# Performance work log

Hardware: AMD Instinct MI355X
Metric: run time of the kernel (lower is better)

## Reference

```python
import jax, jax.numpy as jnp
import numpy as np

B, L, DIM, HEADS = 2, 2048, 1536, 12
HD = DIM // HEADS  # 128
C = HD // 2        # 64 rotary pairs
EPS = 1e-6


def setup_inputs() -> dict:
    key = jax.random.key(0)
    ks = jax.random.split(key, 8)
    x = jax.random.normal(ks[0], (B, L, DIM), jnp.float32)
    # ragged grids: sample0 fills L, sample1 has 2*24*32 = 1536 valid tokens
    grid_sizes = jnp.array([[2, 32, 32], [2, 24, 32]], dtype=jnp.int32)
    seq_lens = jnp.array([2048, 1536], dtype=jnp.int32)
    # rope freqs table [1024, C] (cos/sin of pos * inv_freq)
    pos = jnp.arange(1024, dtype=jnp.float32)[:, None]
    inv = 1.0 / (10000.0 ** (jnp.arange(C, dtype=jnp.float32) / C))
    ang = pos * inv
    freqs_cos, freqs_sin = jnp.cos(ang), jnp.sin(ang)
    init = lambda k: jax.random.normal(k, (DIM, DIM), jnp.float32) / np.sqrt(DIM)
    return dict(
        x=x, seq_lens=seq_lens, grid_sizes=grid_sizes,
        freqs_cos=freqs_cos, freqs_sin=freqs_sin,
        Wq=init(ks[1]), bq=jnp.zeros((DIM,), jnp.float32),
        Wk=init(ks[2]), bk=jnp.zeros((DIM,), jnp.float32),
        Wv=init(ks[3]), bv=jnp.zeros((DIM,), jnp.float32),
        Wo=init(ks[4]), bo=jnp.zeros((DIM,), jnp.float32),
        gq=jnp.ones((DIM,), jnp.float32), gk=jnp.ones((DIM,), jnp.float32),
    )


def _rope_one(xb, grid, cos, sin):
    # xb: [L, n, d]; grid: (f, h, w); cos/sin: [1024, C]
    f, h, w = grid[0], grid[1], grid[2]
    c = cos.shape[1]
    c2 = c // 3
    c1 = c - 2 * c2  # freqs split [c1, c2, c2] over axes (f, h, w)
    p = jnp.arange(xb.shape[0])
    hw = h * w
    valid = p < f * hw
    fi = jnp.where(valid, p // hw, 0)
    hi = jnp.where(valid, (p // w) % h, 0)
    wi = jnp.where(valid, p % w, 0)
    cos_p = jnp.concatenate([cos[fi, :c1], cos[hi, c1:c1 + c2], cos[wi, c1 + c2:]], axis=-1)
    sin_p = jnp.concatenate([sin[fi, :c1], sin[hi, c1:c1 + c2], sin[wi, c1 + c2:]], axis=-1)
    # positions beyond seq_len pass through unrotated (identity rotation)
    cos_p = jnp.where(valid[:, None], cos_p, 1.0)[:, None, :]  # [L,1,C]
    sin_p = jnp.where(valid[:, None], sin_p, 0.0)[:, None, :]
    xr, xi = xb[..., 0::2], xb[..., 1::2]
    out_r = xr * cos_p - xi * sin_p
    out_i = xr * sin_p + xi * cos_p
    return jnp.stack([out_r, out_i], axis=-1).reshape(xb.shape)


_rope_apply = jax.vmap(_rope_one, in_axes=(0, 0, None, None))


def _rms(t, g):
    t32 = t.astype(jnp.float32)
    return (t32 * jax.lax.rsqrt(jnp.mean(t32 * t32, axis=-1, keepdims=True) + EPS) * g).astype(t.dtype)


def reference(x, seq_lens, grid_sizes, freqs_cos, freqs_sin,
              Wq, bq, Wk, bk, Wv, bv, Wo, bo, gq, gk):
    b, s = x.shape[:2]
    n, d = HEADS, HD
    q = _rms(x @ Wq + bq, gq).reshape(b, s, n, d)
    k = _rms(x @ Wk + bk, gk).reshape(b, s, n, d)
    v = (x @ Wv + bv).reshape(b, s, n, d)
    q = _rope_apply(q, grid_sizes, freqs_cos, freqs_sin)
    k = _rope_apply(k, grid_sizes, freqs_cos, freqs_sin)
    scale = 1.0 / np.sqrt(d).astype(np.float32)
    scores = jnp.einsum('bqnd,bknd->bnqk', q, k) * scale
    kmask = jnp.arange(s)[None, :] < seq_lens[:, None]  # [b, s] key validity
    scores = jnp.where(kmask[:, None, None, :], scores, jnp.float32(-1e9))
    attn = jax.nn.softmax(scores, axis=-1)
    out = jnp.einsum('bnqk,bknd->bqnd', attn, v).reshape(b, s, n * d)
    return out @ Wo + bo
```

## Files before the change

kernel.cpp:

```cpp
#include <hip/hip_runtime.h>
#include <hip/hip_bf16.h>

#define DIM   1536
#define HEADS 12
#define HD    128
#define LSEQ  2048
#define NB    2
#define NTOK  (NB*LSEQ)

using f32x4  = __attribute__((ext_vector_type(4))) float;
using f32x16 = __attribute__((ext_vector_type(16))) float;
using s16x8  = __attribute__((ext_vector_type(8))) short;
using u16x4  = __attribute__((ext_vector_type(4))) unsigned short;

__device__ __forceinline__ unsigned short f2bf(float f) {
  unsigned int u = __builtin_bit_cast(unsigned int, f);
  u += 0x7fffu + ((u >> 16) & 1u);
  return (unsigned short)(u >> 16);
}
__device__ __forceinline__ float bf2f(unsigned short u) {
  return __builtin_bit_cast(float, (unsigned int)u << 16);
}
__device__ __forceinline__ unsigned pk2(float a, float b) {
  unsigned r;
  asm("v_cvt_pk_bf16_f32 %0, %1, %2" : "=v"(r) : "v"(a), "v"(b));
  return r;
}
__device__ __forceinline__ unsigned long long pack4bf(float a, float b, float c, float d) {
  return (unsigned long long)f2bf(a) | ((unsigned long long)f2bf(b) << 16) |
         ((unsigned long long)f2bf(c) << 32) | ((unsigned long long)f2bf(d) << 48);
}
__device__ __forceinline__ void plswap(unsigned &x, unsigned &y) {
  asm volatile("v_permlane32_swap_b32 %0, %1" : "+v"(x), "+v"(y));
}
__device__ __forceinline__ void gload_lds16(const void* g, void* l) {
  __builtin_amdgcn_global_load_lds(
      (__attribute__((address_space(1))) void*)const_cast<void*>(g),
      (__attribute__((address_space(3))) void*)l,
      16, 0, 0);
}

__global__ __launch_bounds__(256) void prep(
    const float* __restrict__ x, unsigned short* __restrict__ xb,
    const float* __restrict__ W0, const float* __restrict__ W1,
    const float* __restrict__ W2, const float* __restrict__ W3,
    unsigned short* __restrict__ Wt) {
  __shared__ unsigned short t[64][68];
  const int bid = blockIdx.x;
  const int tid = threadIdx.x;
  if (bid < 2304) {
    const int z = bid / 576, rem = bid % 576;
    const float* W = z == 0 ? W0 : z == 1 ? W1 : z == 2 ? W2 : W3;
    unsigned short* out = Wt + (size_t)z * DIM * DIM;
    const int n0 = (rem % 24) * 64, k0 = (rem / 24) * 64;
#pragma unroll
    for (int i = 0; i < 16; i++) {
      int idx = tid + i * 256;
      int r = idx >> 6, c = idx & 63;
      t[r][c] = f2bf(W[(size_t)(k0 + r) * DIM + n0 + c]);
    }
    __syncthreads();
#pragma unroll
    for (int i = 0; i < 16; i++) {
      int idx = tid + i * 256;
      int r = idx >> 6, c = idx & 63;
      out[(size_t)(n0 + r) * DIM + k0 + c] = t[c][r];
    }
  } else {
    int i = ((bid - 2304) * 256 + tid) * 4;
    int stride = 1024 * 256 * 4;
    for (; i < NTOK * DIM; i += stride) {
      f32x4 v = *(const f32x4*)(x + i);
      u16x4 o;
      o[0] = f2bf(v[0]); o[1] = f2bf(v[1]); o[2] = f2bf(v[2]); o[3] = f2bf(v[3]);
      *(u16x4*)(xb + i) = o;
    }
  }
}

__global__ __launch_bounds__(256) void gemm_bt(
    const unsigned short* __restrict__ A, const unsigned short* __restrict__ Bt,
    void* __restrict__ Cv,
    const float* __restrict__ b0, const float* __restrict__ b1, const float* __restrict__ b2,
    int M, int N, int K, int biasMode, int outBf16) {
  __shared__ __align__(16) unsigned short As[128 * 64];
  __shared__ __align__(16) unsigned short Bs[128 * 64];
  const int tid = threadIdx.x;
  const int lane = tid & 63, w = tid >> 6;
  const int wr = w >> 1, wc = w & 1;
  const int l15 = lane & 15, g4 = lane >> 4;
  const int nwg = gridDim.x * gridDim.y;
  const int bidf = blockIdx.y * gridDim.x + blockIdx.x;
  const int cpx = nwg >> 3;
  const int sw = (bidf & 7) * cpx + (bidf >> 3);
  const int m0 = (sw / gridDim.x) * 128, n0 = (sw % gridDim.x) * 128;

  f32x4 acc[4][4];
#pragma unroll
  for (int i = 0; i < 4; i++)
#pragma unroll
    for (int j = 0; j < 4; j++) acc[i][j] = (f32x4){0.f, 0.f, 0.f, 0.f};

  for (int kt = 0; kt < K; kt += 64) {
    __syncthreads();
#pragma unroll
    for (int i = 0; i < 4; i++) {
      int c = tid + i * 256;
      int row = c >> 3, g = c & 7;
      int gs = g ^ (row & 7);
      gload_lds16(A + (size_t)(m0 + row) * K + kt + gs * 8, As + c * 8);
    }
#pragma unroll
    for (int i = 0; i < 4; i++) {
      int c = tid + i * 256;
      int row = c >> 3, g = c & 7;
      int gs = g ^ (row & 7);
      gload_lds16(Bt + (size_t)(n0 + row) * K + kt + gs * 8, Bs + c * 8);
    }
    __syncthreads();
#pragma unroll
    for (int kk = 0; kk < 2; kk++) {
      s16x8 af[4], bfr[4];
#pragma unroll
      for (int m = 0; m < 4; m++) {
        int row = wr * 64 + m * 16 + l15;
        int off = row * 128 + ((kk * 64 + g4 * 16) ^ ((row & 7) << 4));
        af[m] = *(const s16x8*)((const char*)As + off);
      }
#pragma unroll
      for (int n = 0; n < 4; n++) {
        int row = wc * 64 + n * 16 + l15;
        int off = row * 128 + ((kk * 64 + g4 * 16) ^ ((row & 7) << 4));
        bfr[n] = *(const s16x8*)((const char*)Bs + off);
      }
#pragma unroll
      for (int m = 0; m < 4; m++)
#pragma unroll
        for (int n = 0; n < 4; n++)
          acc[m][n] = __builtin_amdgcn_mfma_f32_16x16x32_bf16(af[m], bfr[n], acc[m][n], 0, 0, 0);
    }
  }
#pragma unroll
  for (int m = 0; m < 4; m++)
#pragma unroll
    for (int n = 0; n < 4; n++)
#pragma unroll
      for (int r = 0; r < 4; r++) {
        int grow = m0 + wr * 64 + m * 16 + g4 * 4 + r;
        int gcol = n0 + wc * 64 + n * 16 + l15;
        float bias = (biasMode == 1)
                         ? b0[gcol]
                         : (gcol < 1536 ? b0[gcol]
                                        : (gcol < 3072 ? b1[gcol - 1536] : b2[gcol - 3072]));
        float val = acc[m][n][r] + bias;
        if (outBf16) ((unsigned short*)Cv)[(size_t)grow * N + gcol] = f2bf(val);
        else         ((float*)Cv)[(size_t)grow * N + gcol] = val;
      }
}

__global__ __launch_bounds__(256) void rmsv(
    const unsigned short* __restrict__ qkvb,
    const float* __restrict__ gq, const float* __restrict__ gk,
    const int* __restrict__ grid_sizes,
    const float* __restrict__ fcos, const float* __restrict__ fsin,
    unsigned short* __restrict__ qb, unsigned short* __restrict__ kb,
    unsigned short* __restrict__ vt) {
  __shared__ float qrow[1536], krow[1536];
  __shared__ float red[8];
  __shared__ unsigned short tile[64][130];
  const int tid = threadIdx.x;
  if (blockIdx.x < 4096) {
    const int t = blockIdx.x;
    const int b = t >> 11, l = t & 2047;
    const unsigned short* rq = qkvb + (size_t)t * 4608;
    const unsigned short* rk = rq + 1536;
    float sq = 0.f, sk = 0.f;
    if (tid < 192) {
      s16x8 vq = *(const s16x8*)(rq + tid * 8);
      s16x8 vk = *(const s16x8*)(rk + tid * 8);
#pragma unroll
      for (int j = 0; j < 8; j++) {
        float a = bf2f((unsigned short)vq[j]); qrow[tid * 8 + j] = a; sq += a * a;
        float c = bf2f((unsigned short)vk[j]); krow[tid * 8 + j] = c; sk += c * c;
      }
    }
    for (int o = 32; o; o >>= 1) { sq += __shfl_down(sq, o); sk += __shfl_down(sk, o); }
    if ((tid & 63) == 0) { red[tid >> 6] = sq; red[4 + (tid >> 6)] = sk; }
    __syncthreads();
    const float rsq = rsqrtf((red[0] + red[1] + red[2] + red[3]) * (1.f / 1536.f) + 1e-6f);
    const float rsk = rsqrtf((red[4] + red[5] + red[6] + red[7]) * (1.f / 1536.f) + 1e-6f);
    const float QS = 0.08838834764831845f * 1.4426950408889634f;
    const int fg = grid_sizes[b * 3 + 0], hg = grid_sizes[b * 3 + 1], wg = grid_sizes[b * 3 + 2];
    const int hw = hg * wg;
    const bool valid = l < fg * hw;
    const int fi = valid ? l / hw : 0;
    const int hi = valid ? (l / wg) % hg : 0;
    const int wi = valid ? l % wg : 0;
    const size_t obase = (((size_t)b * HEADS) * LSEQ + l) * HD;
    for (int i = tid; i < HEADS * 64; i += 256) {
      int hd = i >> 6, j = i & 63;
      float c, s;
      if (valid) {
        int idx = j < 22 ? fi : (j < 43 ? hi : wi);
        c = fcos[idx * 64 + j]; s = fsin[idx * 64 + j];
      } else { c = 1.f; s = 0.f; }
      int col = hd * 128 + 2 * j;
      size_t o = obase + (size_t)hd * LSEQ * HD + 2 * j;
      float xr = qrow[col] * rsq * gq[col];
      float xi = qrow[col + 1] * rsq * gq[col + 1];
      float q0 = (xr * c - xi * s) * QS, q1 = (xr * s + xi * c) * QS;
      *(unsigned int*)(qb + o) = (unsigned int)f2bf(q0) | ((unsigned int)f2bf(q1) << 16);
      xr = krow[col] * rsk * gk[col];
      xi = krow[col + 1] * rsk * gk[col + 1];
      *(unsigned int*)(kb + o) =
          (unsigned int)f2bf(xr * c - xi * s) | ((unsigned int)f2bf(xr * s + xi * c) << 16);
    }
  } else {
    const int r = blockIdx.x - 4096;
    const int lt = r & 31, hb = r >> 5;
    const int h = hb % 12, b = hb / 12;
    const int l0 = lt * 64;
#pragma unroll
    for (int i = 0; i < 4; i++) {
      int idx = tid + i * 256;
      int tk = idx >> 4, dc = (idx & 15) * 8;
      s16x8 v = *(const s16x8*)(qkvb + (size_t)(b * 2048 + l0 + tk) * 4608 + 3072 + h * 128 + dc);
#pragma unroll
      for (int j = 0; j < 8; j++) tile[tk][dc + j] = (unsigned short)v[j];
    }
    __syncthreads();
    const size_t ob = (((size_t)b * HEADS + h) * HD) * LSEQ + l0;
#pragma unroll
    for (int i = 0; i < 4; i++) {
      int idx = tid + i * 256;
      int d = idx >> 3, ck = (idx & 7) * 8;
      s16x8 o;
#pragma unroll
      for (int j = 0; j < 8; j++) o[j] = (short)tile[ck + j][d];
      *(s16x8*)(vt + ob + (size_t)d * LSEQ + ck) = o;
    }
  }
}

__global__ __launch_bounds__(256) void flash(
    const unsigned short* __restrict__ qb, const unsigned short* __restrict__ kb,
    const unsigned short* __restrict__ vt, const int* __restrict__ seq_lens,
    unsigned short* __restrict__ pO, float* __restrict__ pls, float* __restrict__ pm) {
  const int orig = blockIdx.x + 16 * (blockIdx.y + 12 * blockIdx.z);
  const int wg = (orig & 7) * 96 + (orig >> 3);
  const int qt = wg & 15;
  const int r4 = wg >> 4;
  const int hh = r4 % 12;
  const int z2 = r4 / 12;
  const int b = z2 >> 1, half = z2 & 1;
  const int tid = threadIdx.x, lane = tid & 63, w = tid >> 6;
  const int l31 = lane & 31, hi = lane >> 5;
  __shared__ __align__(16) unsigned short Ks[2][32 * 128];
  __shared__ __align__(16) unsigned short Vs[2][128 * 32];
  const size_t bh = (size_t)b * HEADS + hh;
  const int q0 = qt * 128 + w * 32;

  s16x8 qf[8];
  {
    const unsigned short* qp = qb + (bh * LSEQ + q0 + l31) * HD + hi * 8;
#pragma unroll
    for (int s = 0; s < 8; s++) qf[s] = *(const s16x8*)(qp + s * 16);
  }
  const int ntile = seq_lens[b] >> 5;
  const int htiles = ntile >> 1;
  const int k0t = half * htiles;
  const int kend = k0t + htiles;
  asm volatile("s_waitcnt vmcnt(0)" ::: "memory");

  f32x16 acc[4];
#pragma unroll
  for (int d = 0; d < 4; d++)
#pragma unroll
    for (int r = 0; r < 16; r++) acc[d][r] = 0.f;
  float mrow = -1e30f, ls = 0.f;

#define STAGE_K(T, BUF)                                                                \
  _Pragma("unroll") for (int i = 0; i < 2; i++) {                                      \
    int c = tid + i * 256, row = c >> 4, seg = c & 15, ss = seg ^ (row & 15);          \
    gload_lds16(kb + (bh * LSEQ + (T) * 32 + row) * HD + ss * 8, &Ks[BUF][0] + c * 8); \
  }
#define STAGE_V(T, BUF)                                                                \
  _Pragma("unroll") for (int i = 0; i < 2; i++) {                                      \
    int c = tid + i * 256, row = c >> 2, seg = c & 3, ss = seg ^ ((row >> 1) & 3);     \
    gload_lds16(vt + (bh * HD + row) * LSEQ + (T) * 32 + ss * 8, &Vs[BUF][0] + c * 8); \
  }

  STAGE_K(k0t, 0); STAGE_V(k0t, 0);
  STAGE_K(k0t + 1, 1); STAGE_V(k0t + 1, 1);

  for (int kt = k0t; kt < kend; kt++) {
    const int cur = kt & 1;
    asm volatile("s_waitcnt vmcnt(4)" ::: "memory");
    __builtin_amdgcn_s_barrier();
    __builtin_amdgcn_sched_barrier(0);
    f32x16 st0;
#pragma unroll
    for (int r = 0; r < 16; r++) st0[r] = 0.f;
    const char* ksb = (const char*)&Ks[cur][0];
    __builtin_amdgcn_s_setprio(1);
#pragma unroll
    for (int s = 0; s < 8; s++) {
      int g = 2 * s + hi;
      s16x8 kf = *(const s16x8*)(ksb + l31 * 256 + ((g ^ (l31 & 15)) << 4));
      st0 = __builtin_amdgcn_mfma_f32_32x32x16_bf16(kf, qf[s], st0, 0, 0, 0);
    }
    __builtin_amdgcn_s_setprio(0);
    f32x16 mt;
#pragma unroll
    for (int r = 0; r < 16; r++) mt[r] = st0[r];
#pragma unroll
    for (int off = 8; off; off >>= 1)
#pragma unroll
      for (int r = 0; r < off; r++) mt[r] = fmaxf(mt[r], mt[r + off]);
    float mx = fmaxf(mt[0], __shfl_xor(mt[0], 32));
    const bool grow = mx > mrow + 8.0f;
    const float alpha = grow ? exp2f(mrow - mx) : 1.f;
    if (grow) mrow = mx;
#pragma unroll
    for (int r = 0; r < 16; r++) st0[r] = exp2f(st0[r] - mrow);
    f32x16 sm;
#pragma unroll
    for (int r = 0; r < 16; r++) sm[r] = st0[r];
#pragma unroll
    for (int off = 8; off; off >>= 1)
#pragma unroll
      for (int r = 0; r < off; r++) sm[r] += sm[r + off];
    ls = ls * alpha + (sm[0] + __shfl_xor(sm[0], 32));
    if (__any((int)grow)) {
#pragma unroll
      for (int d = 0; d < 4; d++)
#pragma unroll
        for (int r = 0; r < 16; r++) acc[d][r] *= alpha;
    }
    union U { unsigned u[4]; s16x8 v; } pa0, pa1;
    {
      unsigned c0 = pk2(st0[0], st0[1]),  c1 = pk2(st0[2], st0[3]);
      unsigned c2 = pk2(st0[4], st0[5]),  c3 = pk2(st0[6], st0[7]);
      unsigned c4 = pk2(st0[8], st0[9]),  c5 = pk2(st0[10], st0[11]);
      unsigned c6 = pk2(st0[12], st0[13]), c7 = pk2(st0[14], st0[15]);
      plswap(c0, c2); plswap(c1, c3); plswap(c4, c6); plswap(c5, c7);
      pa0.u[0] = c0; pa0.u[1] = c1; pa0.u[2] = c2; pa0.u[3] = c3;
      pa1.u[0] = c4; pa1.u[1] = c5; pa1.u[2] = c6; pa1.u[3] = c7;
    }
    const char* vsb = (const char*)&Vs[cur][0];
    __builtin_amdgcn_s_setprio(1);
#pragma unroll
    for (int slot = 0; slot < 2; slot++) {
      s16x8 pb = slot == 0 ? pa0.v : pa1.v;
      int g = 2 * slot + hi;
#pragma unroll
      for (int d = 0; d < 4; d++) {
        int row = d * 32 + l31;
        s16x8 vf = *(const s16x8*)(vsb + row * 64 + ((g ^ ((row >> 1) & 3)) << 4));
        acc[d] = __builtin_amdgcn_mfma_f32_32x32x16_bf16(vf, pb, acc[d], 0, 0, 0);
      }
    }
    __builtin_amdgcn_s_setprio(0);
    __builtin_amdgcn_s_barrier();
    __builtin_amdgcn_sched_barrier(0);
    {
      int knext = (kt + 2 < kend) ? kt + 2 : kt;
      STAGE_K(knext, cur); STAGE_V(knext, cur);
    }
  }
  asm volatile("s_waitcnt vmcnt(0)" ::: "memory");
#undef STAGE_K
#undef STAGE_V
  const int p = ((b * 12 + hh) * 16 + qt) * 2 + half;
  const int ql = w * 32 + l31;
  unsigned short* pop = pO + ((size_t)p * 128 + ql) * 128 + hi * 4;
#pragma unroll
  for (int d = 0; d < 4; d++)
#pragma unroll
    for (int j = 0; j < 4; j++) {
      unsigned long long pk = pack4bf(acc[d][4 * j], acc[d][4 * j + 1],
                                      acc[d][4 * j + 2], acc[d][4 * j + 3]);
      *(unsigned long long*)(pop + d * 32 + 8 * j) = pk;
    }
  if (hi == 0) {
    pls[(size_t)p * 128 + ql] = ls;
    pm[(size_t)p * 128 + ql] = mrow;
  }
}

__global__ __launch_bounds__(256) void merge(
    const unsigned short* __restrict__ pO, const float* __restrict__ pls,
    const float* __restrict__ pm, unsigned short* __restrict__ ob) {
  const int qt = blockIdx.x, h = blockIdx.y, b = blockIdx.z;
  const int p0 = ((b * 12 + h) * 16 + qt) * 2;
  const int tid = threadIdx.x;
#pragma unroll
  for (int i = tid; i < 2048; i += 256) {
    int q = i >> 4, c = (i & 15) * 8;
    float m0 = pm[(size_t)p0 * 128 + q],  m1 = pm[(size_t)(p0 + 1) * 128 + q];
    float l0 = pls[(size_t)p0 * 128 + q], l1 = pls[(size_t)(p0 + 1) * 128 + q];
    float m = fmaxf(m0, m1);
    float a0 = exp2f(m0 - m), a1 = exp2f(m1 - m);
    float inv = 1.f / (a0 * l0 + a1 * l1);
    a0 *= inv; a1 *= inv;
    s16x8 o0 = *(const s16x8*)(pO + ((size_t)p0 * 128 + q) * 128 + c);
    s16x8 o1 = *(const s16x8*)(pO + ((size_t)(p0 + 1) * 128 + q) * 128 + c);
    s16x8 o;
#pragma unroll
    for (int j = 0; j < 8; j++)
      o[j] = (short)f2bf(bf2f((unsigned short)o0[j]) * a0 + bf2f((unsigned short)o1[j]) * a1);
    *(s16x8*)(ob + ((size_t)(b * LSEQ) + qt * 128 + q) * DIM + h * HD + c) = o;
  }
}

extern "C" void kernel_launch(void* const* d_in, const int* in_sizes, int n_in,
                              void* d_out, int out_size, void* d_ws, size_t ws_size,
                              hipStream_t stream) {
  const float* x    = (const float*)d_in[0];
  const int*   seq  = (const int*)d_in[1];
  const int*   grids= (const int*)d_in[2];
  const float* fcos = (const float*)d_in[3];
  const float* fsin = (const float*)d_in[4];
  const float* Wq   = (const float*)d_in[5];
  const float* bq   = (const float*)d_in[6];
  const float* Wk   = (const float*)d_in[7];
  const float* bk   = (const float*)d_in[8];
  const float* Wv   = (const float*)d_in[9];
  const float* bv   = (const float*)d_in[10];
  const float* Wo   = (const float*)d_in[11];
  const float* bo   = (const float*)d_in[12];
  const float* gq   = (const float*)d_in[13];
  const float* gk   = (const float*)d_in[14];

  char* ws = (char*)d_ws;
  unsigned short* xb   = (unsigned short*)(ws);
  unsigned short* Wt   = (unsigned short*)(ws + 12582912);
  unsigned short* qkvb = (unsigned short*)(ws + 31457280);
  unsigned short* qbb  = (unsigned short*)(ws + 69206016);
  unsigned short* kbb  = (unsigned short*)(ws + 81788928);
  unsigned short* pO   = (unsigned short*)(ws + 31457280);
  float*          pls  = (float*)(ws + 31457280 + 25165824);
  float*          pm   = (float*)(ws + 31457280 + 25165824 + 393216);
  unsigned short* vt   = (unsigned short*)d_out;
  unsigned short* obb  = xb;
  float* out = (float*)d_out;

  prep<<<3328, 256, 0, stream>>>(x, xb, Wq, Wk, Wv, Wo, Wt);
  gemm_bt<<<dim3(36, 32), 256, 0, stream>>>(xb, Wt, qkvb, bq, bk, bv, NTOK, 3 * DIM, DIM, 0, 1);
  rmsv<<<4864, 256, 0, stream>>>(qkvb, gq, gk, grids, fcos, fsin, qbb, kbb, vt);
  flash<<<dim3(16, 12, 4), 256, 0, stream>>>(qbb, kbb, vt, seq, pO, pls, pm);
  merge<<<dim3(16, 12, 2), 256, 0, stream>>>(pO, pls, pm, obb);
  gemm_bt<<<dim3(12, 32), 256, 0, stream>>>(obb, Wt + (size_t)3 * DIM * DIM, out,
                                            bo, bo, bo, NTOK, DIM, DIM, 1, 0);
}
```

Measured before the change: 242.2 us.

## Use 256x256-tile double-buffered GEMM with 512 threads for QKV projection

Adds a new GEMM kernel for the fused QKV projection that computes 256x256 output tiles with 8 waves, K-step 32 and double-buffered LDS loads through direct global-to-LDS copies with XOR swizzling. Larger tiles raise arithmetic intensity and cut global traffic for the 4096x4608x1536 GEMM, and the two-stage prefetch overlaps loads with MFMA. In exchange it launches only 288 workgroups, which may underfill the GPU's CUs, and each thread holds 128 accumulator registers, which limits occupancy.

```diff
diff --git a/kernel.cpp b/kernel.cpp
--- a/kernel.cpp
+++ b/kernel.cpp
@@ -76,6 +76,94 @@
       *(u16x4*)(xb + i) = o;
     }
   }
+}
+
+__global__ __launch_bounds__(512, 4) void gemm256b(
+    const unsigned short* __restrict__ A, const unsigned short* __restrict__ Bt,
+    void* __restrict__ Cv,
+    const float* __restrict__ b0, const float* __restrict__ b1, const float* __restrict__ b2,
+    int M, int N, int K, int biasMode, int outBf16) {
+  __shared__ __align__(16) unsigned short As[2][256 * 32];
+  __shared__ __align__(16) unsigned short Bs[2][256 * 32];
+  const int tid = threadIdx.x;
+  const int lane = tid & 63;
+  const int l15 = lane & 15, g4 = lane >> 4;
+  const int wid = tid >> 6, wr = wid >> 2, wc = wid & 3;
+  const int nwg = gridDim.x * gridDim.y;
+  const int bidf = blockIdx.y * gridDim.x + blockIdx.x;
+  const int cpx = nwg >> 3;
+  const int sw = (bidf & 7) * cpx + (bidf >> 3);
+  const int m0 = (sw / gridDim.x) * 256, n0 = (sw % gridDim.x) * 256;
+
+  f32x4 acc[8][4];
+#pragma unroll
+  for (int i = 0; i < 8; i++)
+#pragma unroll
+    for (int j = 0; j < 4; j++) acc[i][j] = (f32x4){0.f, 0.f, 0.f, 0.f};
+
+#define SG_A(T, BUF)                                                                   \
+  _Pragma("unroll") for (int i = 0; i < 2; i++) {                                      \
+    int cc = tid + i * 512, row = cc >> 2, ch = cc & 3, gs = ch ^ (row & 3);           \
+    gload_lds16(A + (size_t)(m0 + row) * K + (T) * 32 + gs * 8, &As[BUF][0] + cc * 8); \
+  }
+#define SG_B(T, BUF)                                                                   \
+  _Pragma("unroll") for (int i = 0; i < 2; i++) {                                      \
+    int cc = tid + i * 512, row = cc >> 2, ch = cc & 3, gs = ch ^ (row & 3);           \
+    gload_lds16(Bt + (size_t)(n0 + row) * K + (T) * 32 + gs * 8, &Bs[BUF][0] + cc * 8); \
+  }
+#define RD(BASE, R) \
+  (*(const s16x8*)((BASE) + (R) * 64 + ((g4 * 16) ^ (((R) & 3) << 4))))
+
+  const int NT = K >> 5;
+  SG_A(0, 0); SG_B(0, 0);
+  SG_A(1, 1); SG_B(1, 1);
+
+  for (int T = 0; T < NT; T++) {
+    const int cur = T & 1;
+    asm volatile("s_waitcnt vmcnt(4)" ::: "memory");
+    __builtin_amdgcn_s_barrier();
+    __builtin_amdgcn_sched_barrier(0);
+    const char* ab = (const char*)&As[cur][0];
+    const char* bb = (const char*)&Bs[cur][0];
+    s16x8 af[8], bf[4];
+#pragma unroll
+    for (int m = 0; m < 8; m++) { int lr = wr * 128 + m * 16 + l15; af[m] = RD(ab, lr); }
+#pragma unroll
+    for (int n = 0; n < 4; n++) { int rb = wc * 64 + n * 16 + l15; bf[n] = RD(bb, rb); }
+    __builtin_amdgcn_s_setprio(1);
+#pragma unroll
+    for (int m = 0; m < 8; m++)
+#pragma unroll
+      for (int n = 0; n < 4; n++)
+        acc[m][n] = __builtin_amdgcn_mfma_f32_16x16x32_bf16(af[m], bf[n], acc[m][n], 0, 0, 0);
+    __builtin_amdgcn_s_setprio(0);
+    __builtin_amdgcn_s_barrier();
+    __builtin_amdgcn_sched_barrier(0);
+    {
+      int Tn = (T + 2 < NT) ? T + 2 : T;
+      SG_A(Tn, cur); SG_B(Tn, cur);
+    }
+  }
+  asm volatile("s_waitcnt vmcnt(0)" ::: "memory");
+#undef SG_A
+#undef SG_B
+#undef RD
+#pragma unroll
+  for (int m = 0; m < 8; m++)
+#pragma unroll
+    for (int n = 0; n < 4; n++)
+#pragma unroll
+      for (int r = 0; r < 4; r++) {
+        int grow = m0 + wr * 128 + m * 16 + g4 * 4 + r;
+        int gcol = n0 + wc * 64 + n * 16 + l15;
+        float bias = (biasMode == 1)
+                         ? b0[gcol]
+                         : (gcol < 1536 ? b0[gcol]
+                                        : (gcol < 3072 ? b1[gcol - 1536] : b2[gcol - 3072]));
+        float val = acc[m][n][r] + bias;
+        if (outBf16) ((unsigned short*)Cv)[(size_t)grow * N + gcol] = f2bf(val);
+        else         ((float*)Cv)[(size_t)grow * N + gcol] = val;
+      }
 }
 
 __global__ __launch_bounds__(256) void gemm_bt(
@@ -446,7 +534,7 @@
   float* out = (float*)d_out;
 
   prep<<<3328, 256, 0, stream>>>(x, xb, Wq, Wk, Wv, Wo, Wt);
-  gemm_bt<<<dim3(36, 32), 256, 0, stream>>>(xb, Wt, qkvb, bq, bk, bv, NTOK, 3 * DIM, DIM, 0, 1);
+  gemm256b<<<dim3(18, 16), 512, 0, stream>>>(xb, Wt, qkvb, bq, bk, bv, NTOK, 3 * DIM, DIM, 0, 1);
   rmsv<<<4864, 256, 0, stream>>>(qkvb, gq, gk, grids, fcos, fsin, qbb, kbb, vt);
   flash<<<dim3(16, 12, 4), 256, 0, stream>>>(qbb, kbb, vt, seq, pO, pls, pm);
   merge<<<dim3(16, 12, 2), 256, 0, stream>>>(pO, pls, pm, obb);
```

Result: slower. 944.8 us (+290.1%).
